# Optimization experiments

Hardware: AMD Instinct MI355X
Metric: run time of the kernel (lower is better)

Reference implementation:

```python
import jax, jax.numpy as jnp
import numpy as np

B, T, DIN, H = 8, 512, 256, 512
D = 2 * H            # d_model = 1024
HEADS, DH, DEPTH, M = 8, 128, 2, 256  # M = nb_features
FF = 4 * D
KEPS = 1e-4          # performer kernel epsilon


def setup_inputs() -> dict:
    key = jax.random.key(0)
    ks = iter(jax.random.split(key, 64))
    def nrm(shape, s=1.0):
        return jax.random.normal(next(ks), shape, jnp.float32) * s
    inp = {"x": nrm((B, T, DIN))}
    # BiLSTM params, stacked over direction [2, ...]; torch gate order i,f,g,o
    for l, din in ((0, DIN), (1, D)):
        s = 1.0 / np.sqrt(H)
        inp[f"l{l}_Wih"] = nrm((2, 4 * H, din), s)
        inp[f"l{l}_Whh"] = nrm((2, 4 * H, H), s)
        inp[f"l{l}_bih"] = nrm((2, 4 * H), s)
        inp[f"l{l}_bhh"] = nrm((2, 4 * H), s)
    # FAVOR+ random projection (buffer), [nb_features, dim_head]
    inp["proj"] = nrm((M, DH))
    sd = 1.0 / np.sqrt(D)
    inp["ln1_g"] = jnp.ones((DEPTH, D)); inp["ln1_b"] = jnp.zeros((DEPTH, D))
    for n in ("Wq", "Wk", "Wv", "Wo"):
        inp[n] = nrm((DEPTH, D, D), sd)
    for n in ("bq", "bk", "bv", "bo"):
        inp[n] = jnp.zeros((DEPTH, D))
    inp["ln2_g"] = jnp.ones((DEPTH, D)); inp["ln2_b"] = jnp.zeros((DEPTH, D))
    inp["Wf1"] = nrm((DEPTH, D, FF), sd); inp["bf1"] = jnp.zeros((DEPTH, FF))
    inp["Wf2"] = nrm((DEPTH, FF, D), 1.0 / np.sqrt(FF)); inp["bf2"] = jnp.zeros((DEPTH, D))
    inp["cW1"] = nrm((D, H), sd); inp["cb1"] = jnp.zeros((H,))
    inp["cW2"] = nrm((H, 2), 1.0 / np.sqrt(H)); inp["cb2"] = jnp.zeros((2,))
    return inp


def _lstm_dir(x, Wih, Whh, bih, bhh, reverse):
    xs = jnp.swapaxes(x, 0, 1)                      # [T,B,Din]
    h0 = jnp.zeros((x.shape[0], H), x.dtype)
    def step(carry, xt):
        h, c = carry
        z = xt @ Wih.T + h @ Whh.T + bih + bhh      # [B,4H]
        i, f, g, o = jnp.split(z, 4, axis=-1)
        c = jax.nn.sigmoid(f) * c + jax.nn.sigmoid(i) * jnp.tanh(g)
        h = jax.nn.sigmoid(o) * jnp.tanh(c)
        return (h, c), h
    _, hs = jax.lax.scan(step, (h0, h0), xs, reverse=reverse)
    return jnp.swapaxes(hs, 0, 1)                   # [B,T,H], time-aligned


def _bilstm(x, Wih, Whh, bih, bhh):
    fwd = _lstm_dir(x, Wih[0], Whh[0], bih[0], bhh[0], False)
    bwd = _lstm_dir(x, Wih[1], Whh[1], bih[1], bhh[1], True)
    return jnp.concatenate([fwd, bwd], axis=-1)     # [B,T,2H]


def _ln(x, g, b):
    mu = jnp.mean(x, -1, keepdims=True)
    v = jnp.mean((x - mu) ** 2, -1, keepdims=True)
    return (x - mu) * jax.lax.rsqrt(v + 1e-5) * g + b


def _favor(data, proj, is_query):
    # softmax_kernel of performer-pytorch (eval mode, fixed projection)
    dn = DH ** -0.25
    dd = jnp.einsum('bhnd,md->bhnm', data * dn, proj)
    diag = jnp.sum(data * data, -1) * (dn * dn * 0.5)      # [b,h,n]
    if is_query:
        mx = jnp.max(dd, axis=-1, keepdims=True)
    else:
        mx = jnp.max(dd, axis=(-1, -2), keepdims=True)
    return (jnp.exp(dd - diag[..., None] - mx) + KEPS) * (M ** -0.5)


def _heads(x, W, b):
    return (x @ W + b).reshape(B, T, HEADS, DH).transpose(0, 2, 1, 3)


def reference(x, l0_Wih, l0_Whh, l0_bih, l0_bhh, l1_Wih, l1_Whh, l1_bih, l1_bhh,
              proj, ln1_g, ln1_b, Wq, bq, Wk, bk, Wv, bv, Wo, bo,
              ln2_g, ln2_b, Wf1, bf1, Wf2, bf2, cW1, cb1, cW2, cb2):
    h = _bilstm(x, l0_Wih, l0_Whh, l0_bih, l0_bhh)
    h = _bilstm(h, l1_Wih, l1_Whh, l1_bih, l1_bhh)          # [B,T,D]
    for i in range(DEPTH):
        # pre-norm FAVOR+ self-attention, non-causal linear attention
        y = _ln(h, ln1_g[i], ln1_b[i])
        q = _favor(_heads(y, Wq[i], bq[i]), proj, True)     # [b,h,n,m]
        k = _favor(_heads(y, Wk[i], bk[i]), proj, False)
        v = _heads(y, Wv[i], bv[i])                         # [b,h,n,d]
        dinv = 1.0 / jnp.einsum('bhnm,bhm->bhn', q, k.sum(axis=2))
        ctx = jnp.einsum('bhnm,bhnd->bhmd', k, v)
        o = jnp.einsum('bhnm,bhmd->bhnd', q, ctx) * dinv[..., None]
        o = o.transpose(0, 2, 1, 3).reshape(B, T, D)
        h = h + (o @ Wo[i] + bo[i])
        # pre-norm feedforward (GELU, mult 4)
        y = _ln(h, ln2_g[i], ln2_b[i])
        h = h + (jax.nn.gelu(y @ Wf1[i] + bf1[i], approximate=False) @ Wf2[i] + bf2[i])
    pooled = h.mean(axis=1)                                 # [B,D]
    logits = jax.nn.relu(pooled @ cW1 + cb1) @ cW2 + cb2    # [B,2]
    return logits
```

## Files before the change

### kernel.cpp

```cpp
#include <hip/hip_runtime.h>

#define KEPS 1e-4f

typedef __attribute__((ext_vector_type(8))) short bf16x8;
typedef __attribute__((ext_vector_type(4))) float f32x4;
typedef __attribute__((ext_vector_type(4))) unsigned u32x4;
typedef unsigned short u16;

__device__ float g_z0[2u*512*2048*8];
__device__ float g_z1[2u*512*2048*8];
__device__ float g_hres[8u*512*1024];
__device__ float g_qlin[8u*8*512*128];
__device__ float g_klin[8u*8*512*128];
__device__ float g_vlin[8u*8*512*128];
__device__ float g_qp[8u*8*512*256];
__device__ float g_ddb[8u*8*512*256];
__device__ float g_kT[8u*8*256*512];
__device__ float g_ctx[64u*256*128];
__device__ float g_bs0[2*2048];
__device__ float g_bs1[2*2048];
__device__ float g_diagq[32768];
__device__ float g_diagk[32768];
__device__ float g_kmx[64];
__device__ float g_ksum[64*256];
__device__ float g_dinv[32768];
__device__ __align__(16) unsigned g_hbuf[2*2*8*256];
__device__ float g_pooled[8*1024];
__device__ unsigned g_flags[1024];

__device__ u16 g_xbf[8u*512*256];
__device__ u16 g_x1bf[8u*512*1024];
__device__ u16 g_ybf[8u*512*1024];
__device__ u16 g_ylo[8u*512*1024];
__device__ u16 g_obufbf[8u*512*1024];
__device__ u16 g_ffbbf[8u*512*4096];
__device__ u16 g_qhi[8u*8*512*128];
__device__ u16 g_qlo2[8u*8*512*128];
__device__ u16 g_khi[8u*8*512*128];
__device__ u16 g_klo2[8u*8*512*128];
__device__ u16 g_wih0b[2u*2048*256];
__device__ u16 g_wih1b[2u*2048*1024];
__device__ u16 g_wvt[2u*1024*1024];
__device__ u16 g_wot[2u*1024*1024];
__device__ u16 g_wf1t[2u*4096*1024];
__device__ u16 g_wf2t[2u*1024*4096];
__device__ u16 g_wqth[2u*1024*1024];
__device__ u16 g_wqtl[2u*1024*1024];
__device__ u16 g_wkth[2u*1024*1024];
__device__ u16 g_wktl[2u*1024*1024];
__device__ u16 g_projh[256*128];
__device__ u16 g_projl[256*128];

__device__ __forceinline__ float gelu_f(float x) {
  return 0.5f * x * (1.f + erff(x * 0.70710678118654752f));
}
__device__ __forceinline__ unsigned f2bf(float f) {
  unsigned x = __float_as_uint(f);
  return (x + 0x7FFFu + ((x >> 16) & 1u)) >> 16;
}
__device__ __forceinline__ float bf2f(unsigned h) {
  return __uint_as_float(h << 16);
}
__device__ __forceinline__ u32x4 ld16_sc1(const unsigned* p) {
  u32x4 v;
  asm volatile("global_load_dwordx4 %0, %1, off sc1\n\ts_waitcnt vmcnt(0)"
               : "=v"(v) : "v"(p) : "memory");
  return v;
}
__device__ __forceinline__ void st16_sc1(unsigned* p, u32x4 v) {
  asm volatile("global_store_dwordx4 %0, %1, off sc1" :: "v"(p), "v"(v) : "memory");
}
__device__ __forceinline__ void st4_sc1(unsigned* p, unsigned v) {
  asm volatile("global_store_dword %0, %1, off sc1" :: "v"(p), "v"(v) : "memory");
}

__global__ void k_zero(int* p) { p[blockIdx.x*256 + threadIdx.x] = 0; }

__global__ void k_add2(float* __restrict__ dst, const float* __restrict__ a,
                       const float* __restrict__ b, int n) {
  int i = blockIdx.x * 256 + threadIdx.x;
  if (i < n) dst[i] = a[i] + b[i];
}
__global__ void k_cvt(const float* __restrict__ src, u16* __restrict__ dst, int n4) {
  int i = blockIdx.x * 256 + threadIdx.x;
  if (i < n4) {
    float4 v = ((const float4*)src)[i];
    ushort4 o; o.x=(u16)f2bf(v.x); o.y=(u16)f2bf(v.y); o.z=(u16)f2bf(v.z); o.w=(u16)f2bf(v.w);
    ((ushort4*)dst)[i] = o;
  }
}
__global__ void k_scale_split(const float* __restrict__ a, u16* __restrict__ dh,
                              u16* __restrict__ dl, float s, int n) {
  int i = blockIdx.x*256 + threadIdx.x;
  if (i < n) {
    float v = a[i]*s;
    unsigned h = f2bf(v);
    dh[i] = (u16)h; dl[i] = (u16)f2bf(v - bf2f(h));
  }
}
__global__ void k_w2bfT(const float* __restrict__ src, u16* __restrict__ dst,
                        int K, int N, long long sBS, long long dBS)
{
  __shared__ float tile[32][33];
  const int z = blockIdx.z;
  const int n0 = blockIdx.x*32, k0 = blockIdx.y*32;
  const int tx = threadIdx.x, ty = threadIdx.y;
  const float* s = src + (long long)z*sBS;
  u16* d = dst + (long long)z*dBS;
  #pragma unroll
  for (int j = 0; j < 4; ++j)
    tile[ty + j*8][tx] = s[(long long)(k0 + ty + j*8)*N + n0 + tx];
  __syncthreads();
  #pragma unroll
  for (int j = 0; j < 4; ++j)
    d[(long long)(n0 + ty + j*8)*K + k0 + tx] = (u16)f2bf(tile[tx][ty + j*8]);
}
__global__ void k_w2bfT_split(const float* __restrict__ src, u16* __restrict__ dh,
                              u16* __restrict__ dl, int K, int N,
                              long long sBS, long long dBS)
{
  __shared__ float tile[32][33];
  const int z = blockIdx.z;
  const int n0 = blockIdx.x*32, k0 = blockIdx.y*32;
  const int tx = threadIdx.x, ty = threadIdx.y;
  const float* s = src + (long long)z*sBS;
  #pragma unroll
  for (int j = 0; j < 4; ++j)
    tile[ty + j*8][tx] = s[(long long)(k0 + ty + j*8)*N + n0 + tx];
  __syncthreads();
  #pragma unroll
  for (int j = 0; j < 4; ++j) {
    const float v = tile[tx][ty + j*8];
    const unsigned h = f2bf(v);
    const long long off = (long long)z*dBS + (long long)(n0 + ty + j*8)*K + k0 + tx;
    dh[off] = (u16)h; dl[off] = (u16)f2bf(v - bf2f(h));
  }
}

template<int MODE>
__global__ __launch_bounds__(256)
void k_bgemm(const u16* __restrict__ A, const u16* __restrict__ Bw,
             const float* __restrict__ bias, void* __restrict__ Cv,
             int Ndim, int Kdim,
             long long aBS, long long bBS, long long cBS, long long biasBS)
{
  __shared__ __align__(16) u16 As[128*40];
  __shared__ __align__(16) u16 Bs[128*40];
  const int tid = threadIdx.x;
  const int m0 = blockIdx.y * 128, n0 = blockIdx.x * 128, z = blockIdx.z;
  const u16* Ab = A + (long long)z*aBS;
  const u16* Bb = Bw + (long long)z*bBS;
  const int wv = tid >> 6, l = tid & 63;
  const int wm = wv >> 1, wn = wv & 1;
  const int lr = l & 15, lk = l >> 4;
  const int str = tid >> 2, stc = (tid & 3)*8;
  f32x4 acc[4][4];
  #pragma unroll
  for (int i=0;i<4;++i)
    #pragma unroll
    for (int j=0;j<4;++j) acc[i][j] = (f32x4){0.f,0.f,0.f,0.f};

  for (int k0 = 0; k0 < Kdim; k0 += 32) {
    #pragma unroll
    for (int q = 0; q < 2; ++q) {
      const int r = q*64 + str;
      *(uint4*)&As[r*40 + stc] = *(const uint4*)&Ab[(long long)(m0 + r)*Kdim + k0 + stc];
      *(uint4*)&Bs[r*40 + stc] = *(const uint4*)&Bb[(long long)(n0 + r)*Kdim + k0 + stc];
    }
    __syncthreads();
    bf16x8 af[4], bfr[4];
    #pragma unroll
    for (int i=0;i<4;++i) af[i]  = *(bf16x8*)&As[(wm*64 + i*16 + lr)*40 + lk*8];
    #pragma unroll
    for (int j=0;j<4;++j) bfr[j] = *(bf16x8*)&Bs[(wn*64 + j*16 + lr)*40 + lk*8];
    #pragma unroll
    for (int i=0;i<4;++i)
      #pragma unroll
      for (int j=0;j<4;++j)
        acc[i][j] = __builtin_amdgcn_mfma_f32_16x16x32_bf16(af[i], bfr[j], acc[i][j], 0, 0, 0);
    __syncthreads();
  }

  #pragma unroll
  for (int j=0;j<4;++j) {
    const int n = n0 + wn*64 + j*16 + lr;
    const float bvv = bias ? bias[(long long)z*biasBS + n] : 0.f;
    #pragma unroll
    for (int i=0;i<4;++i) {
      #pragma unroll
      for (int r=0;r<4;++r) {
        const int m = m0 + wm*64 + i*16 + lk*4 + r;
        float v = acc[i][j][r] + bvv;
        if (MODE == 0) {
          ((float*)Cv)[(long long)z*cBS + (long long)m*Ndim + n] = v;
        } else if (MODE == 1) {
          const int b_ = m >> 9, t_ = m & 511;
          ((float*)Cv)[(long long)z*cBS + ((long long)t_*2048 + n)*8 + b_] = v;
        } else if (MODE == 2) {
          const int b_ = m >> 9, t_ = m & 511;
          const int hd = n >> 7;
          ((float*)Cv)[(((long long)(b_*8 + hd))*512 + t_)*128 + (n & 127)] = v;
        } else if (MODE == 3) {
          float* cp = (float*)Cv + (long long)m*Ndim + n;
          *cp += v;
        } else if (MODE == 4) {
          ((u16*)Cv)[(long long)m*Ndim + n] = (u16)f2bf(gelu_f(v));
        }
      }
    }
  }
}

template<int MODE>
__global__ __launch_bounds__(256)
void k_b3gemm(const u16* __restrict__ Ah, const u16* __restrict__ Al,
              const u16* __restrict__ Bh, const u16* __restrict__ Bl,
              const float* __restrict__ bias, float* __restrict__ Cf,
              u16* __restrict__ Chi, u16* __restrict__ Clo,
              int Ndim, int Kdim)
{
  __shared__ __align__(16) u16 Ash[128*40];
  __shared__ __align__(16) u16 Asl[128*40];
  __shared__ __align__(16) u16 Bsh[128*40];
  __shared__ __align__(16) u16 Bsl[128*40];
  const int tid = threadIdx.x;
  const int m0 = blockIdx.y * 128, n0 = blockIdx.x * 128;
  const int wv = tid >> 6, l = tid & 63;
  const int wm = wv >> 1, wn = wv & 1;
  const int lr = l & 15, lk = l >> 4;
  const int str = tid >> 2, stc = (tid & 3)*8;
  f32x4 acc[4][4];
  #pragma unroll
  for (int i=0;i<4;++i)
    #pragma unroll
    for (int j=0;j<4;++j) acc[i][j] = (f32x4){0.f,0.f,0.f,0.f};

  for (int k0 = 0; k0 < Kdim; k0 += 32) {
    #pragma unroll
    for (int q = 0; q < 2; ++q) {
      const int r = q*64 + str;
      const long long ao = (long long)(m0 + r)*Kdim + k0 + stc;
      const long long bo = (long long)(n0 + r)*Kdim + k0 + stc;
      *(uint4*)&Ash[r*40 + stc] = *(const uint4*)&Ah[ao];
      *(uint4*)&Asl[r*40 + stc] = *(const uint4*)&Al[ao];
      *(uint4*)&Bsh[r*40 + stc] = *(const uint4*)&Bh[bo];
      *(uint4*)&Bsl[r*40 + stc] = *(const uint4*)&Bl[bo];
    }
    __syncthreads();
    bf16x8 ah[4], al_[4], bh[4], bl_[4];
    #pragma unroll
    for (int i=0;i<4;++i) {
      ah[i]  = *(bf16x8*)&Ash[(wm*64 + i*16 + lr)*40 + lk*8];
      al_[i] = *(bf16x8*)&Asl[(wm*64 + i*16 + lr)*40 + lk*8];
    }
    #pragma unroll
    for (int j=0;j<4;++j) {
      bh[j]  = *(bf16x8*)&Bsh[(wn*64 + j*16 + lr)*40 + lk*8];
      bl_[j] = *(bf16x8*)&Bsl[(wn*64 + j*16 + lr)*40 + lk*8];
    }
    #pragma unroll
    for (int i=0;i<4;++i)
      #pragma unroll
      for (int j=0;j<4;++j) {
        acc[i][j] = __builtin_amdgcn_mfma_f32_16x16x32_bf16(ah[i],  bh[j],  acc[i][j], 0, 0, 0);
        acc[i][j] = __builtin_amdgcn_mfma_f32_16x16x32_bf16(ah[i],  bl_[j], acc[i][j], 0, 0, 0);
        acc[i][j] = __builtin_amdgcn_mfma_f32_16x16x32_bf16(al_[i], bh[j],  acc[i][j], 0, 0, 0);
      }
    __syncthreads();
  }

  #pragma unroll
  for (int j=0;j<4;++j) {
    const int n = n0 + wn*64 + j*16 + lr;
    const float bvv = bias ? bias[n] : 0.f;
    #pragma unroll
    for (int i=0;i<4;++i) {
      #pragma unroll
      for (int r=0;r<4;++r) {
        const int m = m0 + wm*64 + i*16 + lk*4 + r;
        float v = acc[i][j][r] + bvv;
        if (MODE == 0) {
          Cf[(long long)m*Ndim + n] = v;
        } else if (MODE == 2) {
          const int b_ = m >> 9, t_ = m & 511;
          const int hd = n >> 7;
          const long long off = (((long long)(b_*8 + hd))*512 + t_)*128 + (n & 127);
          Cf[off] = v;
          const unsigned h = f2bf(v);
          Chi[off] = (u16)h;
          Clo[off] = (u16)f2bf(v - bf2f(h));
        }
      }
    }
  }
}

template<int BT, int MODE>
__global__ __launch_bounds__(256)
void k_gemm(const float* __restrict__ A, const float* __restrict__ Bw,
            const float* __restrict__ bias, float* __restrict__ C,
            int Mdim, int Ndim, int Kdim,
            long long aBS, long long bBS, long long cBS, long long biasBS,
            const float* __restrict__ aux)
{
  __shared__ float As[16][128];
  __shared__ float Bs[16][128];
  const int tid = threadIdx.x;
  const int tx = tid & 15, ty = tid >> 4;
  const int m0 = blockIdx.y * 128, n0 = blockIdx.x * 128;
  const int z = blockIdx.z;
  const float* Ab = A + (long long)z * aBS;
  const float* Bb = Bw + (long long)z * bBS;
  float acc[8][8] = {};

  for (int k0 = 0; k0 < Kdim; k0 += 16) {
    #pragma unroll
    for (int l0 = 0; l0 < 512; l0 += 256) {
      const int ll = l0 + tid;
      const int r = ll >> 2, kq = (ll & 3) * 4;
      float4 v = *(const float4*)&Ab[(long long)(m0 + r) * Kdim + k0 + kq];
      As[kq+0][r] = v.x; As[kq+1][r] = v.y; As[kq+2][r] = v.z; As[kq+3][r] = v.w;
    }
    if (BT) {
      #pragma unroll
      for (int l0 = 0; l0 < 512; l0 += 256) {
        const int ll = l0 + tid;
        const int r = ll >> 2, kq = (ll & 3) * 4;
        float4 v = *(const float4*)&Bb[(long long)(n0 + r) * Kdim + k0 + kq];
        Bs[kq+0][r] = v.x; Bs[kq+1][r] = v.y; Bs[kq+2][r] = v.z; Bs[kq+3][r] = v.w;
      }
    } else {
      #pragma unroll
      for (int l0 = 0; l0 < 512; l0 += 256) {
        const int ll = l0 + tid;
        const int kr = ll >> 5, n4 = (ll & 31) * 4;
        *(float4*)&Bs[kr][n4] = *(const float4*)&Bb[(long long)(k0 + kr) * Ndim + n0 + n4];
      }
    }
    __syncthreads();
    #pragma unroll
    for (int kk = 0; kk < 16; ++kk) {
      float4 af0 = *(const float4*)&As[kk][ty*4];
      float4 af1 = *(const float4*)&As[kk][64 + ty*4];
      float4 bf0 = *(const float4*)&Bs[kk][tx*4];
      float4 bf1 = *(const float4*)&Bs[kk][64 + tx*4];
      float av[8] = {af0.x,af0.y,af0.z,af0.w,af1.x,af1.y,af1.z,af1.w};
      float bv[8] = {bf0.x,bf0.y,bf0.z,bf0.w,bf1.x,bf1.y,bf1.z,bf1.w};
      #pragma unroll
      for (int i = 0; i < 8; ++i)
        #pragma unroll
        for (int j = 0; j < 8; ++j)
          acc[i][j] = fmaf(av[i], bv[j], acc[i][j]);
    }
    __syncthreads();
  }

  float* Cz = C + (long long)z * cBS;
  #pragma unroll
  for (int i = 0; i < 8; ++i) {
    const int m = m0 + ((i < 4) ? (ty*4 + i) : (64 + ty*4 + (i - 4)));
    #pragma unroll
    for (int jb = 0; jb < 2; ++jb) {
      const int ci = n0 + (jb ? 64 : 0) + tx*4;
      float4 v;
      v.x = acc[i][jb*4+0]; v.y = acc[i][jb*4+1];
      v.z = acc[i][jb*4+2]; v.w = acc[i][jb*4+3];
      if (MODE == 0) {
        *(float4*)&Cz[(long long)m * Ndim + ci] = v;
      } else if (MODE == 5) {
        const int b_ = z >> 3, hd = z & 7;
        const float sc = aux[(long long)z*512 + m];
        u16* Cb = (u16*)C;
        const long long off = ((long long)(b_*512 + m))*1024 + hd*128 + ci;
        Cb[off+0] = (u16)f2bf(v.x*sc);
        Cb[off+1] = (u16)f2bf(v.y*sc);
        Cb[off+2] = (u16)f2bf(v.z*sc);
        Cb[off+3] = (u16)f2bf(v.w*sc);
      }
    }
  }
}

template<int OBF>
__global__ __launch_bounds__(512)
void k_lstm4(const float* __restrict__ Z, const float* __restrict__ Whh,
             float* __restrict__ outf, u16* __restrict__ outb,
             unsigned* __restrict__ hbufU, unsigned* __restrict__ flags)
{
  extern __shared__ char smem[];
  short*          Wl    = (short*)smem;
  short*          hl    = (short*)(smem + 131072);
  float*          gates = (float*)(smem + 139264);
  unsigned short* houts = (unsigned short*)(smem + 143360);

  const int slice = blockIdx.x & 15, dir = blockIdx.x >> 4;
  const int tid = threadIdx.x;
  const int u0 = slice * 32;
  unsigned* selfflag = flags + dir*256 + slice*16;
  const unsigned* peer = flags + dir*256;

  for (int blk = tid; blk < 8192; blk += 512) {
    const int lr2 = blk >> 6, bi = blk & 63;
    const long long src = ((long long)dir*2048 + (lr2>>5)*512 + u0 + (lr2&31))*512 + bi*8;
    float4 w0 = *(const float4*)&Whh[src];
    float4 w1 = *(const float4*)&Whh[src + 4];
    unsigned* dst = (unsigned*)&Wl[lr2*512 + (((bi + lr2) & 63) << 3)];
    dst[0] = f2bf(w0.x) | (f2bf(w0.y) << 16);
    dst[1] = f2bf(w0.z) | (f2bf(w0.w) << 16);
    dst[2] = f2bf(w1.x) | (f2bf(w1.y) << 16);
    dst[3] = f2bf(w1.z) | (f2bf(w1.w) << 16);
  }
  for (int i = tid; i < 2048; i += 512) ((unsigned*)hl)[i] = 0u;

  const int wv = tid >> 6, l = tid & 63;
  const int arow = wv*16 + (l & 15);
  const int bb   = l & 7;
  const int qoff = l >> 4;
  const int jj = tid >> 3, bcomb = tid & 7;
  float cst = 0.f;

  for (int s = 0; s < 512; ++s) {
    const int t = dir ? (511 - s) : s;
    float z0v = 0.f, z1v = 0.f, z2v = 0.f, z3v = 0.f;
    if (tid < 256) {
      const float* zp = Z + (((long long)dir*512 + t)*16384) + (u0 + jj)*8 + bcomb;
      z0v = zp[0]; z1v = zp[4096]; z2v = zp[8192]; z3v = zp[12288];
    }
    if (s > 0) {
      if (tid < 16) {
        const unsigned* fp = peer + tid*16;
        while (__hip_atomic_load(fp, __ATOMIC_RELAXED, __HIP_MEMORY_SCOPE_AGENT) < (unsigned)s) {}
      }
      __syncthreads();
      const unsigned base = ((unsigned)((s & 1)*2 + dir)) * 2048;
      u32x4 v = ld16_sc1(&hbufU[base + tid*4]);
      const int b = tid >> 6, q = tid & 63;
      *(u32x4*)((char*)hl + b*1024 + (((q + b) & 63) << 4)) = v;
    }
    __syncthreads();
    f32x4 acc0 = {0.f,0.f,0.f,0.f}, acc1 = {0.f,0.f,0.f,0.f};
    #pragma unroll
    for (int ks = 0; ks < 8; ++ks) {
      const int qa = (2*ks)*4 + qoff, qb = (2*ks + 1)*4 + qoff;
      bf16x8 a0 = *(bf16x8*)&Wl[arow*512 + (((qa + arow) & 63) << 3)];
      bf16x8 b0 = *(bf16x8*)&hl[bb*512   + (((qa + bb)   & 63) << 3)];
      acc0 = __builtin_amdgcn_mfma_f32_16x16x32_bf16(a0, b0, acc0, 0, 0, 0);
      bf16x8 a1 = *(bf16x8*)&Wl[arow*512 + (((qb + arow) & 63) << 3)];
      bf16x8 b1 = *(bf16x8*)&hl[bb*512   + (((qb + bb)   & 63) << 3)];
      acc1 = __builtin_amdgcn_mfma_f32_16x16x32_bf16(a1, b1, acc1, 0, 0, 0);
    }
    const int bcol = l & 15;
    if (bcol < 8) {
      #pragma unroll
      for (int r = 0; r < 4; ++r)
        gates[(wv*16 + qoff*4 + r)*8 + bcol] = acc0[r] + acc1[r];
    }
    __syncthreads();
    if (tid < 256) {
      const float gi = gates[jj*8        + bcomb] + z0v;
      const float gf = gates[(32+jj)*8   + bcomb] + z1v;
      const float gg = gates[(64+jj)*8   + bcomb] + z2v;
      const float go = gates[(96+jj)*8   + bcomb] + z3v;
      const float ig = 1.f/(1.f + expf(-gi));
      const float fg = 1.f/(1.f + expf(-gf));
      const float og = 1.f/(1.f + expf(-go));
      cst = fg*cst + ig*tanhf(gg);
      const float hv = og*tanhf(cst);
      const unsigned hb = f2bf(hv);
      if (OBF) outb[((long long)(bcomb*512 + t))*1024 + (dir<<9) + u0 + jj] = (u16)hb;
      else     outf[((long long)(bcomb*512 + t))*1024 + (dir<<9) + u0 + jj] = hv;
      houts[bcomb*32 + jj] = (unsigned short)hb;
    }
    __syncthreads();
    if (s != 511) {
      if (tid < 32) {
        const int b = tid >> 2, q4 = tid & 3;
        u32x4 v = *(const u32x4*)&houts[b*32 + q4*8];
        const unsigned base2 = ((unsigned)(((s+1) & 1)*2 + dir)) * 2048;
        st16_sc1(&hbufU[base2 + b*256 + (u0 >> 1) + q4*4], v);
      }
      __syncthreads();
      if (tid == 0) st4_sc1(selfflag, (unsigned)(s + 1));
    }
  }
}

__global__ __launch_bounds__(256)
void k_ln(const float* __restrict__ X, const float* __restrict__ gw,
          const float* __restrict__ bw, u16* __restrict__ Yh, u16* __restrict__ Yl)
{
  const int row = blockIdx.x, tid = threadIdx.x;
  const float* xr = X + (long long)row * 1024;
  float4 v = *(const float4*)&xr[tid*4];
  float s  = v.x + v.y + v.z + v.w;
  float ss = v.x*v.x + v.y*v.y + v.z*v.z + v.w*v.w;
  #pragma unroll
  for (int off = 1; off < 64; off <<= 1) {
    s  += __shfl_xor(s, off, 64);
    ss += __shfl_xor(ss, off, 64);
  }
  __shared__ float rs[4], rss[4];
  const int w = tid >> 6;
  if ((tid & 63) == 0) { rs[w] = s; rss[w] = ss; }
  __syncthreads();
  s  = rs[0] + rs[1] + rs[2] + rs[3];
  ss = rss[0] + rss[1] + rss[2] + rss[3];
  const float mu = s * (1.f/1024.f);
  const float var = ss * (1.f/1024.f) - mu*mu;
  const float rstd = rsqrtf(var + 1e-5f);
  float4 g4 = *(const float4*)&gw[tid*4];
  float4 b4 = *(const float4*)&bw[tid*4];
  float4 o;
  o.x = (v.x - mu)*rstd*g4.x + b4.x;
  o.y = (v.y - mu)*rstd*g4.y + b4.y;
  o.z = (v.z - mu)*rstd*g4.z + b4.z;
  o.w = (v.w - mu)*rstd*g4.w + b4.w;
  ushort4 hh, ll;
  hh.x=(u16)f2bf(o.x); ll.x=(u16)f2bf(o.x - bf2f(f2bf(o.x)));
  hh.y=(u16)f2bf(o.y); ll.y=(u16)f2bf(o.y - bf2f(f2bf(o.y)));
  hh.z=(u16)f2bf(o.z); ll.z=(u16)f2bf(o.z - bf2f(f2bf(o.z)));
  hh.w=(u16)f2bf(o.w); ll.w=(u16)f2bf(o.w - bf2f(f2bf(o.w)));
  *(ushort4*)&Yh[(long long)row*1024 + tid*4] = hh;
  *(ushort4*)&Yl[(long long)row*1024 + tid*4] = ll;
}

__global__ void k_diag(const float* __restrict__ X, float* __restrict__ dout)
{
  const int tid = threadIdx.x;
  const int row = blockIdx.x*4 + (tid >> 6);
  const int lane = tid & 63;
  float2 v = *(const float2*)&X[(long long)row*128 + lane*2];
  float ss = v.x*v.x + v.y*v.y;
  #pragma unroll
  for (int off = 1; off < 64; off <<= 1) ss += __shfl_xor(ss, off, 64);
  if (lane == 0) dout[row] = ss * 0.044194173824159216f;
}

__global__ void k_favq(float* __restrict__ dd, const float* __restrict__ diag)
{
  const int tid = threadIdx.x;
  const int row = blockIdx.x*4 + (tid >> 6);
  const int lane = tid & 63;
  float4 v = *(const float4*)&dd[(long long)row*256 + lane*4];
  float mx = fmaxf(fmaxf(v.x, v.y), fmaxf(v.z, v.w));
  #pragma unroll
  for (int off = 1; off < 64; off <<= 1) mx = fmaxf(mx, __shfl_xor(mx, off, 64));
  const float dg = diag[row];
  float4 o;
  o.x = (expf(v.x - dg - mx) + KEPS)*0.0625f;
  o.y = (expf(v.y - dg - mx) + KEPS)*0.0625f;
  o.z = (expf(v.z - dg - mx) + KEPS)*0.0625f;
  o.w = (expf(v.w - dg - mx) + KEPS)*0.0625f;
  *(float4*)&dd[(long long)row*256 + lane*4] = o;
}

__global__ __launch_bounds__(256)
void k_kmax(const float* __restrict__ dd, float* __restrict__ kmx)
{
  const int bh = blockIdx.x, tid = threadIdx.x;
  const float* p = dd + (long long)bh * 131072;
  float mx = -3.4e38f;
  for (int i = tid*4; i < 131072; i += 1024) {
    float4 v = *(const float4*)&p[i];
    mx = fmaxf(mx, fmaxf(fmaxf(v.x, v.y), fmaxf(v.z, v.w)));
  }
  #pragma unroll
  for (int off = 1; off < 64; off <<= 1) mx = fmaxf(mx, __shfl_xor(mx, off, 64));
  __shared__ float red[4];
  if ((tid & 63) == 0) red[tid >> 6] = mx;
  __syncthreads();
  if (tid == 0) kmx[bh] = fmaxf(fmaxf(red[0], red[1]), fmaxf(red[2], red[3]));
}

__global__ void k_fkT(const float* __restrict__ dd, const float* __restrict__ diag,
                      const float* __restrict__ kmx, float* __restrict__ kT)
{
  __shared__ float tile[32][33];
  const int bh = blockIdx.z;
  const int t0 = blockIdx.x * 32, m0 = blockIdx.y * 32;
  const int tx = threadIdx.x, ty = threadIdx.y;
  const float km = kmx[bh];
  #pragma unroll
  for (int j = 0; j < 4; ++j) {
    const int t = t0 + ty + j*8;
    const float v = dd[((long long)bh*512 + t)*256 + m0 + tx];
    tile[ty + j*8][tx] = (expf(v - diag[bh*512 + t] - km) + KEPS) * 0.0625f;
  }
  __syncthreads();
  #pragma unroll
  for (int j = 0; j < 4; ++j) {
    const int m = m0 + ty + j*8;
    kT[((long long)bh*256 + m)*512 + t0 + tx] = tile[tx][ty + j*8];
  }
}

__global__ void k_ksum(const float* __restrict__ kT, float* __restrict__ ksum)
{
  const int tid = threadIdx.x;
  const int row = blockIdx.x*4 + (tid >> 6);
  const int lane = tid & 63;
  float4 a = *(const float4*)&kT[(long long)row*512 + lane*8];
  float4 b = *(const float4*)&kT[(long long)row*512 + lane*8 + 4];
  float s = a.x+a.y+a.z+a.w + b.x+b.y+b.z+b.w;
  #pragma unroll
  for (int off = 1; off < 64; off <<= 1) s += __shfl_xor(s, off, 64);
  if (lane == 0) ksum[row] = s;
}

__global__ void k_dinv(const float* __restrict__ qp, const float* __restrict__ ksum,
                       float* __restrict__ dinv)
{
  const int tid = threadIdx.x;
  const int row = blockIdx.x*4 + (tid >> 6);
  const int lane = tid & 63;
  const int bh = row >> 9;
  float4 q = *(const float4*)&qp[(long long)row*256 + lane*4];
  float4 k = *(const float4*)&ksum[bh*256 + lane*4];
  float s = q.x*k.x + q.y*k.y + q.z*k.z + q.w*k.w;
  #pragma unroll
  for (int off = 1; off < 64; off <<= 1) s += __shfl_xor(s, off, 64);
  if (lane == 0) dinv[row] = 1.f / s;
}

__global__ void k_pool(const float* __restrict__ h, float* __restrict__ pooled)
{
  const int idx = blockIdx.x * 256 + threadIdx.x;
  const int b = idx >> 10, d = idx & 1023;
  const float* p = h + (long long)b * 524288 + d;
  float s0=0,s1=0,s2=0,s3=0;
  for (int t0 = 0; t0 < 512; t0 += 4) {
    s0 += p[(long long)(t0+0)*1024];
    s1 += p[(long long)(t0+1)*1024];
    s2 += p[(long long)(t0+2)*1024];
    s3 += p[(long long)(t0+3)*1024];
  }
  pooled[idx] = (s0+s1+s2+s3) * (1.f/512.f);
}

__global__ __launch_bounds__(256)
void k_cls(const float* __restrict__ pooled, const float* __restrict__ W1,
           const float* __restrict__ b1, const float* __restrict__ W2,
           const float* __restrict__ b2, float* __restrict__ out)
{
  const int b = blockIdx.x, tid = threadIdx.x;
  __shared__ float pl[1024];
  __shared__ float hd[512];
  *(float4*)&pl[tid*4] = *(const float4*)&pooled[b*1024 + tid*4];
  __syncthreads();
  for (int u = tid; u < 512; u += 256) {
    float acc = b1[u];
    for (int k = 0; k < 1024; ++k) acc = fmaf(pl[k], W1[(long long)k*512 + u], acc);
    hd[u] = fmaxf(acc, 0.f);
  }
  __syncthreads();
  if (tid < 2) {
    float acc = b2[tid];
    for (int k = 0; k < 512; ++k) acc = fmaf(hd[k], W2[k*2 + tid], acc);
    out[b*2 + tid] = acc;
  }
}

static void* symp(const void* s) { void* p = nullptr; (void)hipGetSymbolAddress(&p, s); return p; }

extern "C" void kernel_launch(void* const* d_in, const int* in_sizes, int n_in,
                              void* d_out, int out_size, void* d_ws, size_t ws_size,
                              hipStream_t stream)
{
  (void)in_sizes; (void)n_in; (void)d_ws; (void)ws_size; (void)out_size;
  const float* x     = (const float*)d_in[0];
  const float* l0Wih = (const float*)d_in[1];
  const float* l0Whh = (const float*)d_in[2];
  const float* l0bih = (const float*)d_in[3];
  const float* l0bhh = (const float*)d_in[4];
  const float* l1Wih = (const float*)d_in[5];
  const float* l1Whh = (const float*)d_in[6];
  const float* l1bih = (const float*)d_in[7];
  const float* l1bhh = (const float*)d_in[8];
  const float* proj  = (const float*)d_in[9];
  const float* ln1g  = (const float*)d_in[10];
  const float* ln1b  = (const float*)d_in[11];
  const float* Wq    = (const float*)d_in[12];
  const float* Wk    = (const float*)d_in[13];
  const float* Wv    = (const float*)d_in[14];
  const float* Wo    = (const float*)d_in[15];
  const float* bq    = (const float*)d_in[16];
  const float* bk    = (const float*)d_in[17];
  const float* bv    = (const float*)d_in[18];
  const float* bo    = (const float*)d_in[19];
  const float* ln2g  = (const float*)d_in[20];
  const float* ln2b  = (const float*)d_in[21];
  const float* Wf1   = (const float*)d_in[22];
  const float* bf1   = (const float*)d_in[23];
  const float* Wf2   = (const float*)d_in[24];
  const float* bf2   = (const float*)d_in[25];
  const float* cW1   = (const float*)d_in[26];
  const float* cb1   = (const float*)d_in[27];
  const float* cW2   = (const float*)d_in[28];
  const float* cb2   = (const float*)d_in[29];

  float* z0    = (float*)symp(HIP_SYMBOL(g_z0));
  float* z1    = (float*)symp(HIP_SYMBOL(g_z1));
  float* hres  = (float*)symp(HIP_SYMBOL(g_hres));
  float* qlin  = (float*)symp(HIP_SYMBOL(g_qlin));
  float* klin  = (float*)symp(HIP_SYMBOL(g_klin));
  float* vlin  = (float*)symp(HIP_SYMBOL(g_vlin));
  float* qp    = (float*)symp(HIP_SYMBOL(g_qp));
  float* ddb   = (float*)symp(HIP_SYMBOL(g_ddb));
  float* kT    = (float*)symp(HIP_SYMBOL(g_kT));
  float* ctx   = (float*)symp(HIP_SYMBOL(g_ctx));
  float* bs0   = (float*)symp(HIP_SYMBOL(g_bs0));
  float* bs1   = (float*)symp(HIP_SYMBOL(g_bs1));
  float* diagq = (float*)symp(HIP_SYMBOL(g_diagq));
  float* diagk = (float*)symp(HIP_SYMBOL(g_diagk));
  float* kmx   = (float*)symp(HIP_SYMBOL(g_kmx));
  float* ksum  = (float*)symp(HIP_SYMBOL(g_ksum));
  float* dinv  = (float*)symp(HIP_SYMBOL(g_dinv));
  unsigned* hbuf = (unsigned*)symp(HIP_SYMBOL(g_hbuf));
  float* pooled= (float*)symp(HIP_SYMBOL(g_pooled));
  unsigned* flags = (unsigned*)symp(HIP_SYMBOL(g_flags));
  u16* xbf   = (u16*)symp(HIP_SYMBOL(g_xbf));
  u16* x1bf  = (u16*)symp(HIP_SYMBOL(g_x1bf));
  u16* ybf   = (u16*)symp(HIP_SYMBOL(g_ybf));
  u16* ylo   = (u16*)symp(HIP_SYMBOL(g_ylo));
  u16* obufbf= (u16*)symp(HIP_SYMBOL(g_obufbf));
  u16* ffbbf = (u16*)symp(HIP_SYMBOL(g_ffbbf));
  u16* qhi   = (u16*)symp(HIP_SYMBOL(g_qhi));
  u16* qlo2  = (u16*)symp(HIP_SYMBOL(g_qlo2));
  u16* khi   = (u16*)symp(HIP_SYMBOL(g_khi));
  u16* klo2  = (u16*)symp(HIP_SYMBOL(g_klo2));
  u16* wih0b = (u16*)symp(HIP_SYMBOL(g_wih0b));
  u16* wih1b = (u16*)symp(HIP_SYMBOL(g_wih1b));
  u16* wvt   = (u16*)symp(HIP_SYMBOL(g_wvt));
  u16* wot   = (u16*)symp(HIP_SYMBOL(g_wot));
  u16* wf1t  = (u16*)symp(HIP_SYMBOL(g_wf1t));
  u16* wf2t  = (u16*)symp(HIP_SYMBOL(g_wf2t));
  u16* wqth  = (u16*)symp(HIP_SYMBOL(g_wqth));
  u16* wqtl  = (u16*)symp(HIP_SYMBOL(g_wqtl));
  u16* wkth  = (u16*)symp(HIP_SYMBOL(g_wkth));
  u16* wktl  = (u16*)symp(HIP_SYMBOL(g_wktl));
  u16* projh = (u16*)symp(HIP_SYMBOL(g_projh));
  u16* projl = (u16*)symp(HIP_SYMBOL(g_projl));

  const float dn = 0.29730177875068026f;
  const int LSTM_LDS = 143872;
  (void)hipFuncSetAttribute((const void*)k_lstm4<1>,
                            hipFuncAttributeMaxDynamicSharedMemorySize, LSTM_LDS);
  (void)hipFuncSetAttribute((const void*)k_lstm4<0>,
                            hipFuncAttributeMaxDynamicSharedMemorySize, LSTM_LDS);

  k_zero<<<4, 256, 0, stream>>>((int*)flags);
  k_add2<<<16, 256, 0, stream>>>(bs0, l0bih, l0bhh, 4096);
  k_add2<<<16, 256, 0, stream>>>(bs1, l1bih, l1bhh, 4096);
  k_scale_split<<<128, 256, 0, stream>>>(proj, projh, projl, dn, 32768);

  k_cvt<<<1024, 256, 0, stream>>>(x, xbf, 262144);
  k_cvt<<<1024, 256, 0, stream>>>(l0Wih, wih0b, 262144);
  k_cvt<<<4096, 256, 0, stream>>>(l1Wih, wih1b, 1048576);
  k_w2bfT<<<dim3(32,32,2),  dim3(32,8), 0, stream>>>(Wv,  wvt,  1024, 1024, 1048576LL, 1048576LL);
  k_w2bfT<<<dim3(32,32,2),  dim3(32,8), 0, stream>>>(Wo,  wot,  1024, 1024, 1048576LL, 1048576LL);
  k_w2bfT<<<dim3(128,32,2), dim3(32,8), 0, stream>>>(Wf1, wf1t, 1024, 4096, 4194304LL, 4194304LL);
  k_w2bfT<<<dim3(32,128,2), dim3(32,8), 0, stream>>>(Wf2, wf2t, 4096, 1024, 4194304LL, 4194304LL);
  k_w2bfT_split<<<dim3(32,32,2), dim3(32,8), 0, stream>>>(Wq, wqth, wqtl, 1024, 1024, 1048576LL, 1048576LL);
  k_w2bfT_split<<<dim3(32,32,2), dim3(32,8), 0, stream>>>(Wk, wkth, wktl, 1024, 1024, 1048576LL, 1048576LL);

  k_bgemm<1><<<dim3(16,32,2), 256, 0, stream>>>(xbf, wih0b, bs0, z0,
      2048, 256, 0LL, 524288LL, 8388608LL, 2048LL);
  k_lstm4<1><<<32, 512, LSTM_LDS, stream>>>(z0, l0Whh, nullptr, x1bf, hbuf, flags);
  k_bgemm<1><<<dim3(16,32,2), 256, 0, stream>>>(x1bf, wih1b, bs1, z1,
      2048, 1024, 0LL, 2097152LL, 8388608LL, 2048LL);
  k_lstm4<0><<<32, 512, LSTM_LDS, stream>>>(z1, l1Whh, hres, nullptr, hbuf, flags + 512);

  for (int i = 0; i < 2; ++i) {
    const long long wOffU = (long long)i * 1048576;
    k_ln<<<4096, 256, 0, stream>>>(hres, ln1g + i*1024, ln1b + i*1024, ybf, ylo);
    k_b3gemm<2><<<dim3(8,32,1), 256, 0, stream>>>(ybf, ylo, wqth + wOffU, wqtl + wOffU,
        bq + i*1024, qlin, qhi, qlo2, 1024, 1024);
    k_b3gemm<2><<<dim3(8,32,1), 256, 0, stream>>>(ybf, ylo, wkth + wOffU, wktl + wOffU,
        bk + i*1024, klin, khi, klo2, 1024, 1024);
    k_bgemm<2><<<dim3(8,32,1), 256, 0, stream>>>(ybf, wvt + wOffU, bv + i*1024, vlin,
        1024, 1024, 0LL, 0LL, 0LL, 0LL);
    k_diag<<<8192, 256, 0, stream>>>(qlin, diagq);
    k_diag<<<8192, 256, 0, stream>>>(klin, diagk);
    k_b3gemm<0><<<dim3(2,256,1), 256, 0, stream>>>(qhi, qlo2, projh, projl,
        nullptr, qp, nullptr, nullptr, 256, 128);
    k_favq<<<8192, 256, 0, stream>>>(qp, diagq);
    k_b3gemm<0><<<dim3(2,256,1), 256, 0, stream>>>(khi, klo2, projh, projl,
        nullptr, ddb, nullptr, nullptr, 256, 128);
    k_kmax<<<64, 256, 0, stream>>>(ddb, kmx);
    k_fkT<<<dim3(16,8,64), dim3(32,8), 0, stream>>>(ddb, diagk, kmx, kT);
    k_ksum<<<4096, 256, 0, stream>>>(kT, ksum);
    k_gemm<0,0><<<dim3(1,2,64), 256, 0, stream>>>(kT, vlin, nullptr, ctx,
        256, 128, 512, 131072LL, 65536LL, 32768LL, 0LL, nullptr);
    k_dinv<<<8192, 256, 0, stream>>>(qp, ksum, dinv);
    k_gemm<0,5><<<dim3(1,4,64), 256, 0, stream>>>(qp, ctx, nullptr, (float*)obufbf,
        512, 128, 256, 131072LL, 32768LL, 0LL, 0LL, dinv);
    k_bgemm<3><<<dim3(8,32,1), 256, 0, stream>>>(obufbf, wot + wOffU, bo + i*1024, hres,
        1024, 1024, 0LL, 0LL, 0LL, 0LL);
    k_ln<<<4096, 256, 0, stream>>>(hres, ln2g + i*1024, ln2b + i*1024, ybf, ylo);
    k_bgemm<4><<<dim3(32,32,1), 256, 0, stream>>>(ybf, wf1t + (long long)i*4194304,
        bf1 + i*4096, ffbbf, 4096, 1024, 0LL, 0LL, 0LL, 0LL);
    k_bgemm<3><<<dim3(8,32,1), 256, 0, stream>>>(ffbbf, wf2t + (long long)i*4194304,
        bf2 + i*1024, hres, 1024, 4096, 0LL, 0LL, 0LL, 0LL);
  }

  k_pool<<<32, 256, 0, stream>>>(hres, pooled);
  k_cls<<<8, 256, 0, stream>>>(pooled, cW1, cb1, cW2, cb2, (float*)d_out);
}
```

Measured before the change: 4.621 ms.

## Replace LSTM step flags with tags embedded in exchanged hidden-state data

The cross-block handoff of the recurrent hidden state no longer uses separate per-slice flag counters plus an extra barrier and flag store. Instead, a rolling 3-bit step tag is written into the low mantissa bits of the bf16 h values in each 16-byte packet. Every thread spins on its own packet until the expected tag shows up. This takes a polling round trip, a barrier and the flag-zeroing kernel off each serial timestep. In exchange it slightly perturbs some hidden-state values, and correctness relies on stale tags in the reused double buffer never matching the expected ones.

```diff
diff --git a/kernel.cpp b/kernel.cpp
--- a/kernel.cpp
+++ b/kernel.cpp
@@ -26,7 +26,6 @@
 __device__ float g_dinv[32768];
 __device__ __align__(16) unsigned g_hbuf[2*2*8*256];
 __device__ float g_pooled[8*1024];
-__device__ unsigned g_flags[1024];
 
 __device__ u16 g_xbf[8u*512*256];
 __device__ u16 g_x1bf[8u*512*1024];
@@ -70,11 +69,6 @@
 __device__ __forceinline__ void st16_sc1(unsigned* p, u32x4 v) {
   asm volatile("global_store_dwordx4 %0, %1, off sc1" :: "v"(p), "v"(v) : "memory");
 }
-__device__ __forceinline__ void st4_sc1(unsigned* p, unsigned v) {
-  asm volatile("global_store_dword %0, %1, off sc1" :: "v"(p), "v"(v) : "memory");
-}
-
-__global__ void k_zero(int* p) { p[blockIdx.x*256 + threadIdx.x] = 0; }
 
 __global__ void k_add2(float* __restrict__ dst, const float* __restrict__ a,
                        const float* __restrict__ b, int n) {
@@ -383,9 +377,9 @@
 
 template<int OBF>
 __global__ __launch_bounds__(512)
-void k_lstm4(const float* __restrict__ Z, const float* __restrict__ Whh,
+void k_lstm5(const float* __restrict__ Z, const float* __restrict__ Whh,
              float* __restrict__ outf, u16* __restrict__ outb,
-             unsigned* __restrict__ hbufU, unsigned* __restrict__ flags)
+             unsigned* __restrict__ hbufU)
 {
   extern __shared__ char smem[];
   short*          Wl    = (short*)smem;
@@ -396,8 +390,6 @@
   const int slice = blockIdx.x & 15, dir = blockIdx.x >> 4;
   const int tid = threadIdx.x;
   const int u0 = slice * 32;
-  unsigned* selfflag = flags + dir*256 + slice*16;
-  const unsigned* peer = flags + dir*256;
 
   for (int blk = tid; blk < 8192; blk += 512) {
     const int lr2 = blk >> 6, bi = blk & 63;
@@ -418,6 +410,8 @@
   const int qoff = l >> 4;
   const int jj = tid >> 3, bcomb = tid & 7;
   float cst = 0.f;
+  int gt = 1;
+  int pt = 2;
 
   for (int s = 0; s < 512; ++s) {
     const int t = dir ? (511 - s) : s;
@@ -427,13 +421,14 @@
       z0v = zp[0]; z1v = zp[4096]; z2v = zp[8192]; z3v = zp[12288];
     }
     if (s > 0) {
-      if (tid < 16) {
-        const unsigned* fp = peer + tid*16;
-        while (__hip_atomic_load(fp, __ATOMIC_RELAXED, __HIP_MEMORY_SCOPE_AGENT) < (unsigned)s) {}
+      const unsigned base = ((unsigned)((s & 1)*2 + dir)) * 2048;
+      const unsigned* src = &hbufU[base + tid*4];
+      u32x4 v;
+      for (;;) {
+        v = ld16_sc1(src);
+        const int tag = (int)((v.x & 1u) | (((v.x >> 16) & 1u) << 1) | ((v.y & 1u) << 2));
+        if (tag == gt) break;
       }
-      __syncthreads();
-      const unsigned base = ((unsigned)((s & 1)*2 + dir)) * 2048;
-      u32x4 v = ld16_sc1(&hbufU[base + tid*4]);
       const int b = tid >> 6, q = tid & 63;
       *(u32x4*)((char*)hl + b*1024 + (((q + b) & 63) << 4)) = v;
     }
@@ -472,16 +467,16 @@
       houts[bcomb*32 + jj] = (unsigned short)hb;
     }
     __syncthreads();
-    if (s != 511) {
-      if (tid < 32) {
-        const int b = tid >> 2, q4 = tid & 3;
-        u32x4 v = *(const u32x4*)&houts[b*32 + q4*8];
-        const unsigned base2 = ((unsigned)(((s+1) & 1)*2 + dir)) * 2048;
-        st16_sc1(&hbufU[base2 + b*256 + (u0 >> 1) + q4*4], v);
-      }
-      __syncthreads();
-      if (tid == 0) st4_sc1(selfflag, (unsigned)(s + 1));
-    }
+    if (s != 511 && tid < 32) {
+      const int b = tid >> 2, q4 = tid & 3;
+      u32x4 w = *(const u32x4*)&houts[b*32 + q4*8];
+      w.x = (w.x & ~0x00010001u) | (unsigned)(pt & 1) | (((unsigned)(pt >> 1) & 1u) << 16);
+      w.y = (w.y & ~1u) | ((unsigned)(pt >> 2) & 1u);
+      const unsigned base2 = ((unsigned)(((s+1) & 1)*2 + dir)) * 2048;
+      st16_sc1(&hbufU[base2 + b*256 + (u0 >> 1) + q4*4], w);
+    }
+    gt = (gt == 7) ? 1 : gt + 1;
+    pt = (pt == 7) ? 1 : pt + 1;
   }
 }
 
@@ -717,7 +712,6 @@
   float* dinv  = (float*)symp(HIP_SYMBOL(g_dinv));
   unsigned* hbuf = (unsigned*)symp(HIP_SYMBOL(g_hbuf));
   float* pooled= (float*)symp(HIP_SYMBOL(g_pooled));
-  unsigned* flags = (unsigned*)symp(HIP_SYMBOL(g_flags));
   u16* xbf   = (u16*)symp(HIP_SYMBOL(g_xbf));
   u16* x1bf  = (u16*)symp(HIP_SYMBOL(g_x1bf));
   u16* ybf   = (u16*)symp(HIP_SYMBOL(g_ybf));
@@ -743,12 +737,11 @@
 
   const float dn = 0.29730177875068026f;
   const int LSTM_LDS = 143872;
-  (void)hipFuncSetAttribute((const void*)k_lstm4<1>,
+  (void)hipFuncSetAttribute((const void*)k_lstm5<1>,
                             hipFuncAttributeMaxDynamicSharedMemorySize, LSTM_LDS);
-  (void)hipFuncSetAttribute((const void*)k_lstm4<0>,
+  (void)hipFuncSetAttribute((const void*)k_lstm5<0>,
                             hipFuncAttributeMaxDynamicSharedMemorySize, LSTM_LDS);
 
-  k_zero<<<4, 256, 0, stream>>>((int*)flags);
   k_add2<<<16, 256, 0, stream>>>(bs0, l0bih, l0bhh, 4096);
   k_add2<<<16, 256, 0, stream>>>(bs1, l1bih, l1bhh, 4096);
   k_scale_split<<<128, 256, 0, stream>>>(proj, projh, projl, dn, 32768);
@@ -765,10 +758,10 @@
 
   k_bgemm<1><<<dim3(16,32,2), 256, 0, stream>>>(xbf, wih0b, bs0, z0,
       2048, 256, 0LL, 524288LL, 8388608LL, 2048LL);
-  k_lstm4<1><<<32, 512, LSTM_LDS, stream>>>(z0, l0Whh, nullptr, x1bf, hbuf, flags);
+  k_lstm5<1><<<32, 512, LSTM_LDS, stream>>>(z0, l0Whh, nullptr, x1bf, hbuf);
   k_bgemm<1><<<dim3(16,32,2), 256, 0, stream>>>(x1bf, wih1b, bs1, z1,
       2048, 1024, 0LL, 2097152LL, 8388608LL, 2048LL);
-  k_lstm4<0><<<32, 512, LSTM_LDS, stream>>>(z1, l1Whh, hres, nullptr, hbuf, flags + 512);
+  k_lstm5<0><<<32, 512, LSTM_LDS, stream>>>(z1, l1Whh, hres, nullptr, hbuf);
 
   for (int i = 0; i < 2; ++i) {
     const long long wOffU = (long long)i * 1048576;
```

Result: faster. 4.362 ms (-5.6%).
